# Optimization experiments

Hardware: AMD Instinct MI355X
Metric: run time of the kernel (lower is better)

## Reference

```python
import jax, jax.numpy as jnp
import numpy as np

B, L, HS, NWRD, NTGT, DIM = 8, 128, 1024, 32000, 2000, 128
EPS = 1e-12
T = 1.0  # eval temperature


def setup_inputs() -> dict:
    key = jax.random.key(0)
    ks = jax.random.split(key, 16)
    s = 0.02
    return {
        "inp_word": jax.random.randint(ks[0], (B, L), 0, NWRD, dtype=jnp.int32),
        "masks": jnp.ones((B, L), jnp.float32),
        "spt_mask": jax.random.randint(ks[1], (B, L), 0, 2, dtype=jnp.int32),
        "tgt_ids": jnp.sort(jax.random.randint(ks[2], (NTGT,), 0, NWRD, dtype=jnp.int32)),
        "ctx": jax.random.normal(ks[3], (B, L, HS), jnp.float32),
        "W_spt": jax.random.normal(ks[4], (HS, NTGT), jnp.float32) * s,
        "b_spt": jnp.zeros((NTGT,), jnp.float32),
        "W_nrm": jax.random.normal(ks[5], (HS, NWRD), jnp.float32) * s,
        "b_nrm": jnp.zeros((NWRD,), jnp.float32),
        "W_cpy": jax.random.normal(ks[6], (HS, HS), jnp.float32) * s,
        "b_cpy": jnp.zeros((HS,), jnp.float32),
        "word_emb": jax.random.normal(ks[7], (NWRD, DIM), jnp.float32) * s,
        "word_emb_tgt": jax.random.normal(ks[8], (NTGT, DIM), jnp.float32) * s,
        "g_spt": jax.random.gumbel(ks[9], (B, L, NTGT), jnp.float32),
        "g_nrm": jax.random.gumbel(ks[10], (B, L, NWRD + 1), jnp.float32),
    }


def reference(inp_word, masks, spt_mask, tgt_ids, ctx, W_spt, b_spt, W_nrm, b_nrm,
              W_cpy, b_cpy, word_emb, word_emb_tgt, g_spt, g_nrm):
    spt = spt_mask.astype(jnp.float32)                       # keyword tokens
    nrm = (1.0 - spt) * masks                                # normal (non-pad) tokens

    # special-token head: log(softmax + eps)
    pspt = jnp.log(jax.nn.softmax(jnp.einsum('blh,ht->blt', ctx, W_spt) + b_spt, axis=-1) + EPS)

    # normal head: vocab logits + self copy-attention score
    logits_nrm = jnp.einsum('blh,hv->blv', ctx, W_nrm) + b_nrm           # [B,L,NWRD]
    pcpy = jnp.einsum('blh,blh->bl', jnp.einsum('blh,hk->blk', ctx, W_cpy) + b_cpy, ctx)
    pnrm = jnp.log(jax.nn.softmax(jnp.concatenate([logits_nrm, pcpy[..., None]], axis=-1), axis=-1) + EPS)

    # gumbel-softmax relaxed samples
    sft_spt = jax.nn.softmax((pspt + g_spt) / T, axis=-1)    # [B,L,NTGT]
    sft_nrm = jax.nn.softmax((pnrm + g_nrm) / T, axis=-1)    # [B,L,NWRD+1]

    # hard word choices
    yspt = tgt_ids[jnp.argmax(sft_spt, axis=-1)]
    ynrm_raw = jnp.argmax(sft_nrm, axis=-1).astype(jnp.int32)
    ynrm = jnp.where(ynrm_raw == NWRD, inp_word, ynrm_raw)   # copy fallback
    obf_word = jnp.where(spt > 0, yspt, jnp.where(nrm > 0, ynrm, inp_word))

    # blended embeddings, scatter-combined per token group
    spt_emb = jnp.einsum('blt,td->bld', sft_spt, word_emb_tgt)
    nrm_emb = word_emb[inp_word] * sft_nrm[..., -1:] \
        + jnp.einsum('blv,vd->bld', sft_nrm[..., :-1], word_emb)
    base_emb = word_emb[obf_word]
    obf_word_emb = jnp.where(spt[..., None] > 0, spt_emb,
                             jnp.where(nrm[..., None] > 0, nrm_emb, base_emb))
    return obf_word_emb, obf_word, spt
```

## Files before the change

### kernel.cpp

```cpp
#include <hip/hip_runtime.h>
#include <math.h>

#define TOK   1024
#define HSZ   1024
#define DIM   128
#define NWRDC 32000
#define NTGTC 2000

typedef __attribute__((ext_vector_type(8))) short bf16x8;
typedef __attribute__((ext_vector_type(4))) float f32x4;

__device__ __forceinline__ ushort f2bf(float x) {
    union { float f; uint u; } c; c.f = x;
    return (ushort)((c.u + 0x7fffu + ((c.u >> 16) & 1u)) >> 16);
}
__device__ __forceinline__ float bf2f(ushort h) {
    union { uint u; float f; } c; c.u = ((uint)h) << 16;
    return c.f;
}
__device__ __forceinline__ uint4 pk8(const ushort v[8]) {
    uint4 u;
    u.x = (uint)v[0] | ((uint)v[1] << 16);
    u.y = (uint)v[2] | ((uint)v[3] << 16);
    u.z = (uint)v[4] | ((uint)v[5] << 16);
    u.w = (uint)v[6] | ((uint)v[7] << 16);
    return u;
}

#define GLL16(SRC, DST) __builtin_amdgcn_global_load_lds( \
    (const __attribute__((address_space(1))) void*)(SRC), \
    (__attribute__((address_space(3))) void*)(DST), 16, 0, 0)

__global__ __launch_bounds__(256) void split_ctx3(
    const float* __restrict__ x, ushort* __restrict__ hp,
    ushort* __restrict__ mp, ushort* __restrict__ lp)
{
    const int i4 = (blockIdx.x * 256 + threadIdx.x) * 4;
    float4 v = *(const float4*)(x + i4);
    float xs[4] = {v.x, v.y, v.z, v.w};
    ushort hh[4], mm[4], ll[4];
    #pragma unroll
    for (int k = 0; k < 4; ++k) {
        ushort h = f2bf(xs[k]);
        float r1 = xs[k] - bf2f(h);
        ushort m = f2bf(r1);
        ushort l = f2bf(r1 - bf2f(m));
        hh[k] = h; mm[k] = m; ll[k] = l;
    }
    uint2 u;
    u.x = (uint)hh[0] | ((uint)hh[1] << 16); u.y = (uint)hh[2] | ((uint)hh[3] << 16);
    *(uint2*)(hp + i4) = u;
    u.x = (uint)mm[0] | ((uint)mm[1] << 16); u.y = (uint)mm[2] | ((uint)mm[3] << 16);
    *(uint2*)(mp + i4) = u;
    u.x = (uint)ll[0] | ((uint)ll[1] << 16); u.y = (uint)ll[2] | ((uint)ll[3] << 16);
    *(uint2*)(lp + i4) = u;
}

__global__ __launch_bounds__(256, 2) void gemm_cpy(
    const ushort* __restrict__ ahi, const ushort* __restrict__ amd,
    const ushort* __restrict__ alo, const float* __restrict__ W,
    float* __restrict__ C)
{
    __shared__ __align__(16) ushort sm[30720];
    ushort* Ah = sm;
    ushort* Am = sm + 5120;
    ushort* Al = sm + 10240;
    ushort* Bh = sm + 15360;
    ushort* Bm = sm + 20480;
    ushort* Bl = sm + 25600;

    const int tid  = threadIdx.x;
    const int lane = tid & 63;
    const int fr   = lane & 15;
    const int fg   = lane >> 4;
    const int w    = tid >> 6;
    const int wrow = w >> 1;
    const int wcol = w & 1;
    const int t0   = blockIdx.x * 128;
    const int c0   = blockIdx.y * 128;

    const int arow = tid >> 2, akc = tid & 3;
    const int bcol = tid & 127, bkc0 = tid >> 7;

    f32x4 zero4 = {0.f, 0.f, 0.f, 0.f};
    f32x4 acc[4][4];
    #pragma unroll
    for (int i = 0; i < 4; ++i)
        #pragma unroll
        for (int j = 0; j < 4; ++j) acc[i][j] = zero4;

    for (int h0 = 0; h0 < HSZ; h0 += 32) {
        uint4 aH[2], aM[2], aL[2];
        float bx[2][8];
        #pragma unroll
        for (int rr = 0; rr < 2; ++rr) {
            const size_t so = (size_t)(t0 + arow + rr * 64) * HSZ + h0 + akc * 8;
            aH[rr] = *(const uint4*)(ahi + so);
            aM[rr] = *(const uint4*)(amd + so);
            aL[rr] = *(const uint4*)(alo + so);
        }
        #pragma unroll
        for (int rr = 0; rr < 2; ++rr) {
            const int kc = bkc0 + rr * 2;
            const float* wp = W + (size_t)(h0 + kc * 8) * HSZ + c0 + bcol;
            #pragma unroll
            for (int j = 0; j < 8; ++j) bx[rr][j] = wp[(size_t)j * HSZ];
        }
        __syncthreads();
        #pragma unroll
        for (int rr = 0; rr < 2; ++rr) {
            const int row = arow + rr * 64;
            *(uint4*)(Ah + row * 40 + akc * 8) = aH[rr];
            *(uint4*)(Am + row * 40 + akc * 8) = aM[rr];
            *(uint4*)(Al + row * 40 + akc * 8) = aL[rr];
        }
        #pragma unroll
        for (int rr = 0; rr < 2; ++rr) {
            const int kc = bkc0 + rr * 2;
            ushort hh[8], mm[8], ll[8];
            #pragma unroll
            for (int j = 0; j < 8; ++j) {
                float x = bx[rr][j];
                ushort h = f2bf(x);
                float r1 = x - bf2f(h);
                ushort m = f2bf(r1);
                hh[j] = h; mm[j] = m; ll[j] = f2bf(r1 - bf2f(m));
            }
            *(uint4*)(Bh + bcol * 40 + kc * 8) = pk8(hh);
            *(uint4*)(Bm + bcol * 40 + kc * 8) = pk8(mm);
            *(uint4*)(Bl + bcol * 40 + kc * 8) = pk8(ll);
        }
        __syncthreads();
        bf16x8 a1[4], a2[4], a3[4];
        #pragma unroll
        for (int i = 0; i < 4; ++i) {
            const int row = wrow * 64 + i * 16 + fr;
            a1[i] = *(const bf16x8*)(Ah + row * 40 + fg * 8);
            a2[i] = *(const bf16x8*)(Am + row * 40 + fg * 8);
            a3[i] = *(const bf16x8*)(Al + row * 40 + fg * 8);
        }
        #pragma unroll
        for (int j = 0; j < 4; ++j) {
            const int cr = wcol * 64 + j * 16 + fr;
            bf16x8 b1 = *(const bf16x8*)(Bh + cr * 40 + fg * 8);
            bf16x8 b2 = *(const bf16x8*)(Bm + cr * 40 + fg * 8);
            bf16x8 b3 = *(const bf16x8*)(Bl + cr * 40 + fg * 8);
            #pragma unroll
            for (int i = 0; i < 4; ++i) {
                acc[i][j] = __builtin_amdgcn_mfma_f32_16x16x32_bf16(a1[i], b1, acc[i][j], 0, 0, 0);
                acc[i][j] = __builtin_amdgcn_mfma_f32_16x16x32_bf16(a1[i], b2, acc[i][j], 0, 0, 0);
                acc[i][j] = __builtin_amdgcn_mfma_f32_16x16x32_bf16(a2[i], b1, acc[i][j], 0, 0, 0);
                acc[i][j] = __builtin_amdgcn_mfma_f32_16x16x32_bf16(a1[i], b3, acc[i][j], 0, 0, 0);
                acc[i][j] = __builtin_amdgcn_mfma_f32_16x16x32_bf16(a3[i], b1, acc[i][j], 0, 0, 0);
                acc[i][j] = __builtin_amdgcn_mfma_f32_16x16x32_bf16(a2[i], b2, acc[i][j], 0, 0, 0);
            }
        }
    }
    #pragma unroll
    for (int i = 0; i < 4; ++i)
        #pragma unroll
        for (int j = 0; j < 4; ++j)
            #pragma unroll
            for (int r = 0; r < 4; ++r) {
                const int trow = wrow * 64 + i * 16 + fg * 4 + r;
                const int dd   = wcol * 64 + j * 16 + fr;
                C[(size_t)(t0 + trow) * HSZ + c0 + dd] = acc[i][j][r];
            }
}

__global__ __launch_bounds__(256) void pcpy_dot(
    const float* __restrict__ C, const float* __restrict__ ctx,
    const float* __restrict__ bc, float* __restrict__ out)
{
    const int t = blockIdx.x, tid = threadIdx.x;
    const float4 c4 = *(const float4*)(C + (size_t)t * HSZ + tid * 4);
    const float4 x4 = *(const float4*)(ctx + (size_t)t * HSZ + tid * 4);
    const float4 b4 = *(const float4*)(bc + tid * 4);
    float p = (c4.x + b4.x) * x4.x + (c4.y + b4.y) * x4.y
            + (c4.z + b4.z) * x4.z + (c4.w + b4.w) * x4.w;
    #pragma unroll
    for (int off = 32; off > 0; off >>= 1) p += __shfl_down(p, off, 64);
    __shared__ float r4[4];
    if ((tid & 63) == 0) r4[tid >> 6] = p;
    __syncthreads();
    if (tid == 0) out[t] = r4[0] + r4[1] + r4[2] + r4[3];
}

__global__ __launch_bounds__(256, 2) void head_mfma(
    const ushort* __restrict__ ctx_hi, const ushort* __restrict__ ctx_lo,
    const float* __restrict__ W, const float* __restrict__ bias,
    const float* __restrict__ g, const float* __restrict__ emb,
    int V, int ldg, int tps, int n_tiles,
    float* __restrict__ wsW, float* __restrict__ wsBV,
    int* __restrict__ wsBI, float* __restrict__ wsE)
{
    __shared__ __align__(16) char smem[56320];
    ushort* Pl = (ushort*)smem;
    ushort* EM = (ushort*)(smem + 34816);
    float* sm_wsum = (float*)(smem + 53248);
    float* sm_bval = (float*)(smem + 54272);
    int*   sm_bidx = (int*)(smem + 55296);

    const int tid  = threadIdx.x;
    const int lane = tid & 63;
    const int fr   = lane & 15;
    const int fg   = lane >> 4;
    const int wv   = tid >> 6;
    const int wrow = wv >> 1;
    const int wcol = wv & 1;
    const int split = (int)blockIdx.x;
    const int t0    = (int)blockIdx.y * 128;

    if (tid < 128) {
        sm_wsum[tid * 2] = 0.f;        sm_wsum[tid * 2 + 1] = 0.f;
        sm_bval[tid * 2] = -INFINITY;  sm_bval[tid * 2 + 1] = -INFINITY;
        sm_bidx[tid * 2] = 0;          sm_bidx[tid * 2 + 1] = 0;
    }

    const int chunkRd  = (((fr & 1) << 2) | fg) ^ ((fr >> 1) & 7);
    const int laneAoff = wrow * 4096 + (fr >> 1) * 128 + chunkRd * 16;
    const int laneBoff = wcol * 4096 + (fr >> 1) * 128 + chunkRd * 16;

    const int cfA   = (lane & 7) ^ (lane >> 3);
    const int glTok = (wv * 8 + (lane >> 3)) * 2 + (cfA >> 2);
    const int glK   = (cfA & 3) * 8;
    const int glDst = wv * 1024;

    const int c4 = (tid & 31) * 4;
    const int hb = (tid >> 5) * 2;
    int wb01[4], wb23[4];
    #pragma unroll
    for (int i = 0; i < 4; ++i) {
        const int col = c4 + i;
        const int pair = col >> 1;
        const int ch01 = (((col & 1) << 2) | (hb >> 3)) ^ (pair & 7);
        const int ch23 = (((col & 1) << 2) | (2 + (hb >> 3))) ^ (pair & 7);
        wb01[i] = pair * 128 + ch01 * 16 + (hb & 7) * 2;
        wb23[i] = pair * 128 + ch23 * 16 + (hb & 7) * 2;
    }

    f32x4 zero4 = {0.f, 0.f, 0.f, 0.f};
    f32x4 Eacc[4][4];
    #pragma unroll
    for (int i = 0; i < 4; ++i)
        #pragma unroll
        for (int j = 0; j < 4; ++j) Eacc[i][j] = zero4;

    int tbeg = split * tps;
    int tend = tbeg + tps; if (tend > n_tiles) tend = n_tiles;

    #define STAGE_A(STEP, BASE) do {                                              \
        const size_t ro_ = (size_t)(t0 + glTok) * HSZ + (size_t)(STEP) * 32 + glK; \
        GLL16(ctx_hi + ro_,          (BASE) + glDst);                              \
        GLL16(ctx_hi + ro_ + 65536,  (BASE) + 4096 + glDst);                       \
        GLL16(ctx_lo + ro_,          (BASE) + 8192 + glDst);                       \
        GLL16(ctx_lo + ro_ + 65536,  (BASE) + 12288 + glDst);                      \
    } while (0)

    #define LOAD_W(STEP, VV) do {                                                 \
        const int gc_ = c0 + c4;                                                  \
        if (gc_ + 3 < V) {                                                        \
            const float* p_ = W + (size_t)((STEP) * 32 + hb) * V + gc_;           \
            VV[0] = *(const float4*)p_;                                           \
            VV[1] = *(const float4*)(p_ + V);                                     \
            VV[2] = *(const float4*)(p_ + 16 * (size_t)V);                        \
            VV[3] = *(const float4*)(p_ + 17 * (size_t)V);                        \
        } else {                                                                  \
            float4 z_ = {0.f, 0.f, 0.f, 0.f};                                     \
            VV[0] = z_; VV[1] = z_; VV[2] = z_; VV[3] = z_;                       \
        }                                                                         \
    } while (0)

    #define CONV_W(VV) do {                                                       \
        _Pragma("unroll")                                                         \
        for (int i_ = 0; i_ < 4; ++i_) {                                          \
            const float* fv0 = (const float*)&VV[0];                              \
            const float* fv1 = (const float*)&VV[1];                              \
            const float* fv2 = (const float*)&VV[2];                              \
            const float* fv3 = (const float*)&VV[3];                              \
            float a0 = fv0[i_], a1 = fv1[i_], a2 = fv2[i_], a3 = fv3[i_];         \
            ushort h0b = f2bf(a0); ushort l0b = f2bf(a0 - bf2f(h0b));             \
            ushort h1b = f2bf(a1); ushort l1b = f2bf(a1 - bf2f(h1b));             \
            ushort h2b = f2bf(a2); ushort l2b = f2bf(a2 - bf2f(h2b));             \
            ushort h3b = f2bf(a3); ushort l3b = f2bf(a3 - bf2f(h3b));             \
            *(uint*)(smem + 32768 + wb01[i_]) = (uint)h0b | ((uint)h1b << 16);    \
            *(uint*)(smem + 32768 + wb23[i_]) = (uint)h2b | ((uint)h3b << 16);    \
            *(uint*)(smem + 40960 + wb01[i_]) = (uint)l0b | ((uint)l1b << 16);    \
            *(uint*)(smem + 40960 + wb23[i_]) = (uint)l2b | ((uint)l3b << 16);    \
        }                                                                         \
    } while (0)

    for (int tt = tbeg; tt < tend; ++tt) {
        const int c0 = tt * 128;
        f32x4 acc[4][4];
        #pragma unroll
        for (int i = 0; i < 4; ++i)
            #pragma unroll
            for (int j = 0; j < 4; ++j) acc[i][j] = zero4;

        STAGE_A(0, smem);
        {
            float4 v0[4];
            LOAD_W(0, v0);
            CONV_W(v0);
        }
        __syncthreads();

        for (int ks = 0; ks < 32; ++ks) {
            const int cur = ks & 1;
            const bool more = (ks + 1) < 32;
            float4 vn[4];
            if (more) {
                STAGE_A(ks + 1, smem + (cur ^ 1) * 16384);
                LOAD_W(ks + 1, vn);
            }
            char* bA = smem + cur * 16384;
            bf16x8 ah[4], al[4];
            #pragma unroll
            for (int i = 0; i < 4; ++i) {
                ah[i] = *(const bf16x8*)(bA + laneAoff + i * 1024);
                al[i] = *(const bf16x8*)(bA + 8192 + laneAoff + i * 1024);
            }
            #pragma unroll
            for (int j = 0; j < 4; ++j) {
                bf16x8 vbh = *(const bf16x8*)(smem + 32768 + laneBoff + j * 1024);
                bf16x8 vbl = *(const bf16x8*)(smem + 40960 + laneBoff + j * 1024);
                #pragma unroll
                for (int i = 0; i < 4; ++i) {
                    acc[i][j] = __builtin_amdgcn_mfma_f32_16x16x32_bf16(ah[i], vbh, acc[i][j], 0, 0, 0);
                    acc[i][j] = __builtin_amdgcn_mfma_f32_16x16x32_bf16(ah[i], vbl, acc[i][j], 0, 0, 0);
                    acc[i][j] = __builtin_amdgcn_mfma_f32_16x16x32_bf16(al[i], vbh, acc[i][j], 0, 0, 0);
                }
            }
            __syncthreads();
            if (more) {
                CONV_W(vn);
            }
            __syncthreads();
        }

        float bias4[4];
        #pragma unroll
        for (int j = 0; j < 4; ++j) {
            const int gc = c0 + wcol * 64 + j * 16 + fr;
            bias4[j] = (gc < V) ? bias[gc] : 0.f;
        }
        #pragma unroll
        for (int i = 0; i < 4; ++i) {
            #pragma unroll
            for (int r = 0; r < 4; ++r) {
                const int trow = wrow * 64 + i * 16 + fg * 4 + r;
                const float* gp = g + (size_t)(t0 + trow) * ldg + c0 + wcol * 64 + fr;
                float esum = 0.f, mx = -INFINITY;
                int mi = 0;
                #pragma unroll
                for (int j = 0; j < 4; ++j) {
                    const int gc = c0 + wcol * 64 + j * 16 + fr;
                    float e = 0.f;
                    if (gc < V) {
                        const float s = acc[i][j][r] + bias4[j] + gp[j * 16];
                        e = __expf(s);
                        esum += e;
                        if (s > mx) { mx = s; mi = gc; }
                    }
                    Pl[trow * 136 + wcol * 64 + j * 16 + fr] = f2bf(e);
                }
                #pragma unroll
                for (int off = 1; off < 16; off <<= 1) {
                    const float ov = __shfl_xor(mx, off, 64);
                    const int   oi = __shfl_xor(mi, off, 64);
                    esum += __shfl_xor(esum, off, 64);
                    if (ov > mx || (ov == mx && oi < mi)) { mx = ov; mi = oi; }
                }
                if (fr == 0) {
                    sm_wsum[trow * 2 + wcol] += esum;
                    const float cb = sm_bval[trow * 2 + wcol];
                    const int   ci = sm_bidx[trow * 2 + wcol];
                    if (mx > cb || (mx == cb && mi < ci)) {
                        sm_bval[trow * 2 + wcol] = mx;
                        sm_bidx[trow * 2 + wcol] = mi;
                    }
                }
            }
        }

        #pragma unroll
        for (int hf = 0; hf < 2; ++hf) {
            __syncthreads();
            #pragma unroll
            for (int rr = 0; rr < 4; ++rr) {
                const int task = tid + rr * 256;
                const int d = task & 127;
                const int cc = task >> 7;
                ushort o8[8];
                #pragma unroll
                for (int j = 0; j < 8; ++j) {
                    const int gc = c0 + hf * 64 + cc * 8 + j;
                    o8[j] = (gc < V) ? f2bf(emb[(size_t)gc * DIM + d]) : (ushort)0;
                }
                *(uint4*)(EM + d * 72 + cc * 8) = pk8(o8);
            }
            __syncthreads();
            #pragma unroll
            for (int ksb = 0; ksb < 2; ++ksb) {
                bf16x8 ap[4];
                #pragma unroll
                for (int i = 0; i < 4; ++i) {
                    const int row = wrow * 64 + i * 16 + fr;
                    ap[i] = *(const bf16x8*)(Pl + row * 136 + hf * 64 + ksb * 32 + fg * 8);
                }
                #pragma unroll
                for (int j = 0; j < 4; ++j) {
                    const int dd = wcol * 64 + j * 16 + fr;
                    bf16x8 eb = *(const bf16x8*)(EM + dd * 72 + ksb * 32 + fg * 8);
                    #pragma unroll
                    for (int i = 0; i < 4; ++i)
                        Eacc[i][j] = __builtin_amdgcn_mfma_f32_16x16x32_bf16(ap[i], eb, Eacc[i][j], 0, 0, 0);
                }
            }
        }
        __syncthreads();
    }

    __syncthreads();
    if (tid < 128) {
        const float wsv = sm_wsum[tid * 2] + sm_wsum[tid * 2 + 1];
        const float b0 = sm_bval[tid * 2], b1 = sm_bval[tid * 2 + 1];
        const int   i0 = sm_bidx[tid * 2], i1 = sm_bidx[tid * 2 + 1];
        float bv; int bi;
        if (b0 > b1 || (b0 == b1 && i0 < i1)) { bv = b0; bi = i0; }
        else                                   { bv = b1; bi = i1; }
        const size_t o = (size_t)split * TOK + t0 + tid;
        wsW[o] = wsv; wsBV[o] = bv; wsBI[o] = bi;
    }
    #pragma unroll
    for (int i = 0; i < 4; ++i)
        #pragma unroll
        for (int j = 0; j < 4; ++j)
            #pragma unroll
            for (int r = 0; r < 4; ++r) {
                const int trow = wrow * 64 + i * 16 + fg * 4 + r;
                const int dd   = wcol * 64 + j * 16 + fr;
                wsE[((size_t)split * TOK + t0 + trow) * DIM + dd] = Eacc[i][j][r];
            }
}

__global__ __launch_bounds__(128) void combine_kernel(
    const int* __restrict__ inp_word, const float* __restrict__ masks,
    const int* __restrict__ spt_mask, const int* __restrict__ tgt_ids,
    const float* __restrict__ word_emb, const float* __restrict__ pcpy,
    const float* __restrict__ g_nrm,
    const float* __restrict__ nW, const float* __restrict__ nBV,
    const int* __restrict__ nBI, const float* __restrict__ nE, int NVn,
    const float* __restrict__ sW, const float* __restrict__ sBV,
    const int* __restrict__ sBI, const float* __restrict__ sE, int NVs,
    float* __restrict__ out)
{
    const int t = (int)blockIdx.x;
    const int d = (int)threadIdx.x;

    float Wn = 0.f, En = 0.f, bv = -INFINITY; int bi = 0;
    for (int v = 0; v < NVn; ++v) {
        const size_t o = (size_t)v * TOK + t;
        Wn += nW[o];
        En += nE[o * DIM + d];
        const float vv = nBV[o]; const int ii = nBI[o];
        if (vv > bv || (vv == bv && ii < bi)) { bv = vv; bi = ii; }
    }
    const int iw = inp_word[t];
    const float sc = pcpy[t] + g_nrm[(size_t)t * (NWRDC + 1) + NWRDC];
    const float ec = __expf(sc);
    Wn += ec;
    En += ec * word_emb[(size_t)iw * DIM + d];
    const int ynrm = (sc > bv) ? iw : bi;

    float Ws = 0.f, Ese = 0.f, sv = -INFINITY; int si = 0;
    for (int v = 0; v < NVs; ++v) {
        const size_t o = (size_t)v * TOK + t;
        Ws += sW[o];
        Ese += sE[o * DIM + d];
        const float vv = sBV[o]; const int ii = sBI[o];
        if (vv > sv || (vv == sv && ii < si)) { sv = vv; si = ii; }
    }
    const int yspt = tgt_ids[si];

    const float sptf = (float)spt_mask[t];
    const float nrmf = (1.f - sptf) * masks[t];

    float eo; int obf;
    if (sptf > 0.f)      { eo = Ese / Ws; obf = yspt; }
    else if (nrmf > 0.f) { eo = En / Wn;  obf = ynrm; }
    else                 { obf = iw; eo = word_emb[(size_t)iw * DIM + d]; }

    out[(size_t)t * DIM + d] = eo;
    if (d == 0) {
        out[(size_t)TOK * DIM + t]       = (float)obf;
        out[(size_t)TOK * DIM + TOK + t] = sptf;
    }
}

extern "C" void kernel_launch(void* const* d_in, const int* in_sizes, int n_in,
                              void* d_out, int out_size, void* d_ws, size_t ws_size,
                              hipStream_t stream)
{
    const int*   inp_word = (const int*)d_in[0];
    const float* masks    = (const float*)d_in[1];
    const int*   spt_mask = (const int*)d_in[2];
    const int*   tgt_ids  = (const int*)d_in[3];
    const float* ctx      = (const float*)d_in[4];
    const float* W_spt    = (const float*)d_in[5];
    const float* b_spt    = (const float*)d_in[6];
    const float* W_nrm    = (const float*)d_in[7];
    const float* b_nrm    = (const float*)d_in[8];
    const float* W_cpy    = (const float*)d_in[9];
    const float* b_cpy    = (const float*)d_in[10];
    const float* word_emb = (const float*)d_in[11];
    const float* word_emb_tgt = (const float*)d_in[12];
    const float* g_spt    = (const float*)d_in[13];
    const float* g_nrm    = (const float*)d_in[14];
    float* out = (float*)d_out;

    char* wsb = (char*)d_ws;
    float*  pcpy = (float*)wsb;
    ushort* ctxh = (ushort*)(wsb + 4096);
    ushort* ctxm = (ushort*)(wsb + 4096 + 2097152);
    ushort* ctxl = (ushort*)(wsb + 4096 + 4194304);
    char*   region = wsb + 4096 + 6291456;
    float*  Cws = (float*)region;

    const size_t per_split = (size_t)TOK * (DIM + 3) * 4;
    size_t avail = (ws_size > 6295552) ? (ws_size - 6295552) / per_split : 0;
    int NVn, NVs;
    if      (avail >= 72) { NVn = 64; NVs = 8; }
    else if (avail >= 56) { NVn = 48; NVs = 8; }
    else if (avail >= 40) { NVn = 32; NVs = 8; }
    else if (avail >= 24) { NVn = 16; NVs = 8; }
    else if (avail >= 12) { NVn = 8;  NVs = 4; }
    else if (avail >= 3)  { NVn = (int)avail - 1; NVs = 1; }
    else                  { NVn = 1;  NVs = 1; }

    float* nW  = (float*)region;
    float* nBV = nW + (size_t)NVn * TOK;
    int*   nBI = (int*)(nBV + (size_t)NVn * TOK);
    float* nE  = (float*)(nBI + (size_t)NVn * TOK);
    float* sW  = nE + (size_t)NVn * TOK * DIM;
    float* sBV = sW + (size_t)NVs * TOK;
    int*   sBI = (int*)(sBV + (size_t)NVs * TOK);
    float* sE  = (float*)(sBI + (size_t)NVs * TOK);

    const int ntile_n = NWRDC / 128;
    const int tps_n = (ntile_n + NVn - 1) / NVn;
    const int ntile_s = (NTGTC + 127) / 128;
    const int tps_s = (ntile_s + NVs - 1) / NVs;

    split_ctx3<<<dim3(TOK * HSZ / 1024), dim3(256), 0, stream>>>(ctx, ctxh, ctxm, ctxl);
    gemm_cpy<<<dim3(8, 8), dim3(256), 0, stream>>>(ctxh, ctxm, ctxl, W_cpy, Cws);
    pcpy_dot<<<dim3(TOK), dim3(256), 0, stream>>>(Cws, ctx, b_cpy, pcpy);
    head_mfma<<<dim3(NVn, 8), dim3(256), 0, stream>>>(
        ctxh, ctxm, W_nrm, b_nrm, g_nrm, word_emb, NWRDC, NWRDC + 1,
        tps_n, ntile_n, nW, nBV, nBI, nE);
    head_mfma<<<dim3(NVs, 8), dim3(256), 0, stream>>>(
        ctxh, ctxm, W_spt, b_spt, g_spt, word_emb_tgt, NTGTC, NTGTC,
        tps_s, ntile_s, sW, sBV, sBI, sE);
    combine_kernel<<<dim3(TOK), dim3(128), 0, stream>>>(
        inp_word, masks, spt_mask, tgt_ids, word_emb, pcpy, g_nrm,
        nW, nBV, nBI, nE, NVn, sW, sBV, sBI, sE, NVs, out);
    (void)in_sizes; (void)n_in; (void)out_size;
}
```

Baseline: 827.7 us.

## Pre-transpose vocab weights to bf16 and rescore top-3 candidates exactly

Adds a conversion kernel that transposes W_nrm and W_spt into bf16 hi (and lo residual) buffers in workspace. The main head kernel now runs a single-pass bf16 MFMA GEMM, loading both operands directly into LDS instead of converting fp32 weights inside the loop. To recover argmax accuracy it tracks the top-3 candidates per token, and the combine kernel rescores them in double precision using the hi/lo split. This cuts the per-tile weight conversion and the split-precision MFMA work, at the cost of a large workspace and an extra conversion pass over the weights on every call.

```diff
diff --git a/kernel.cpp b/kernel.cpp
--- a/kernel.cpp
+++ b/kernel.cpp
@@ -25,6 +25,15 @@
     u.z = (uint)v[4] | ((uint)v[5] << 16);
     u.w = (uint)v[6] | ((uint)v[7] << 16);
     return u;
+}
+__device__ __forceinline__ void ins3(float v, int ix, float s[3], int ii[3]) {
+    if (v > s[0] || (v == s[0] && ix < ii[0])) {
+        s[2] = s[1]; ii[2] = ii[1]; s[1] = s[0]; ii[1] = ii[0]; s[0] = v; ii[0] = ix;
+    } else if (v > s[1] || (v == s[1] && ix < ii[1])) {
+        s[2] = s[1]; ii[2] = ii[1]; s[1] = v; ii[1] = ix;
+    } else if (v > s[2] || (v == s[2] && ix < ii[2])) {
+        s[2] = v; ii[2] = ix;
+    }
 }
 
 #define GLL16(SRC, DST) __builtin_amdgcn_global_load_lds( \
@@ -54,6 +63,35 @@
     *(uint2*)(mp + i4) = u;
     u.x = (uint)ll[0] | ((uint)ll[1] << 16); u.y = (uint)ll[2] | ((uint)ll[3] << 16);
     *(uint2*)(lp + i4) = u;
+}
+
+__global__ __launch_bounds__(256) void conv_wt(
+    const float* __restrict__ W, int V,
+    ushort* __restrict__ Wh, void* __restrict__ Wl, int lf32)
+{
+    const int col = blockIdx.x * 256 + threadIdx.x;
+    const int k0 = blockIdx.y * 128;
+    for (int kk = 0; kk < 128; kk += 8) {
+        ushort h8[8], l8[8]; float lf[8];
+        #pragma unroll
+        for (int q = 0; q < 8; ++q) {
+            float x = (col < V) ? W[(size_t)(k0 + kk + q) * V + col] : 0.f;
+            union { float f; uint u; } c; c.f = x;
+            ushort h = (ushort)(c.u >> 16);
+            union { uint u; float f; } th; th.u = (uint)h << 16;
+            float r = x - th.f;
+            h8[q] = h; lf[q] = r; l8[q] = f2bf(r);
+        }
+        *(uint4*)(Wh + (size_t)col * 1024 + k0 + kk) = pk8(h8);
+        if (lf32) {
+            float* wl = (float*)Wl + (size_t)col * 1024 + k0 + kk;
+            float4 a = {lf[0], lf[1], lf[2], lf[3]};
+            float4 b = {lf[4], lf[5], lf[6], lf[7]};
+            *(float4*)wl = a; *(float4*)(wl + 4) = b;
+        } else {
+            *(uint4*)((ushort*)Wl + (size_t)col * 1024 + k0 + kk) = pk8(l8);
+        }
+    }
 }
 
 __global__ __launch_bounds__(256, 2) void gemm_cpy(
@@ -186,7 +224,230 @@
     if (tid == 0) out[t] = r4[0] + r4[1] + r4[2] + r4[3];
 }
 
-__global__ __launch_bounds__(256, 2) void head_mfma(
+__global__ __launch_bounds__(256, 2) void head_pre(
+    const ushort* __restrict__ ctx_hi, const ushort* __restrict__ Wt,
+    const float* __restrict__ bias, const float* __restrict__ g,
+    const float* __restrict__ emb,
+    int V, int ldg, int tps, int n_tiles,
+    float* __restrict__ wsW, float* __restrict__ wsBV,
+    int* __restrict__ wsBI, float* __restrict__ wsE)
+{
+    __shared__ __align__(16) char smem[60416];
+    ushort* Pl = (ushort*)smem;
+    ushort* EM = (ushort*)(smem + 34816);
+    float* sm_wsum = (float*)(smem + 53248);
+    float* sm_bval = (float*)(smem + 54272);
+    int*   sm_bidx = (int*)(smem + 57344);
+
+    const int tid  = threadIdx.x;
+    const int lane = tid & 63;
+    const int fr   = lane & 15;
+    const int fg   = lane >> 4;
+    const int wv   = tid >> 6;
+    const int wrow = wv >> 1;
+    const int wcol = wv & 1;
+    const int split = (int)blockIdx.x;
+    const int t0    = (int)blockIdx.y * 128;
+
+    if (tid < 128) {
+        sm_wsum[tid * 2] = 0.f; sm_wsum[tid * 2 + 1] = 0.f;
+        #pragma unroll
+        for (int s = 0; s < 3; ++s) {
+            sm_bval[(tid * 2) * 3 + s] = -INFINITY;
+            sm_bval[(tid * 2 + 1) * 3 + s] = -INFINITY;
+            sm_bidx[(tid * 2) * 3 + s] = 0;
+            sm_bidx[(tid * 2 + 1) * 3 + s] = 0;
+        }
+    }
+
+    const int chunkRd0 = (((fr & 1) << 2) | fg) ^ ((fr >> 1) & 7);
+    int aRd[4], bRd[4];
+    #pragma unroll
+    for (int i = 0; i < 4; ++i) {
+        aRd[i] = wrow * 4096 + i * 1024 + (fr >> 1) * 128 + ((chunkRd0 ^ i) << 4);
+        bRd[i] = wcol * 4096 + i * 1024 + (fr >> 1) * 128 + ((chunkRd0 ^ i) << 4);
+    }
+
+    const int v_ = (lane & 7) ^ (lane >> 3) ^ (wv & 3);
+    int rowq[2];
+    #pragma unroll
+    for (int q = 0; q < 2; ++q)
+        rowq[q] = 2 * (q * 32 + wv * 8 + (lane >> 3)) + (v_ >> 2);
+    const int glK = (v_ & 3) * 8;
+    const size_t srcA0 = (size_t)(t0 + rowq[0]) * HSZ + glK;
+    const size_t srcA1 = (size_t)(t0 + rowq[1]) * HSZ + glK;
+    const int dA0 = wv * 1024, dA1 = 4096 + wv * 1024;
+
+    f32x4 zero4 = {0.f, 0.f, 0.f, 0.f};
+    f32x4 Eacc[4][4];
+    #pragma unroll
+    for (int i = 0; i < 4; ++i)
+        #pragma unroll
+        for (int j = 0; j < 4; ++j) Eacc[i][j] = zero4;
+
+    int tbeg = split * tps;
+    int tend = tbeg + tps; if (tend > n_tiles) tend = n_tiles;
+
+    for (int tt = tbeg; tt < tend; ++tt) {
+        const int c0 = tt * 128;
+        const size_t srcB0 = (size_t)(c0 + rowq[0]) * HSZ + glK;
+        const size_t srcB1 = (size_t)(c0 + rowq[1]) * HSZ + glK;
+        f32x4 acc[4][4];
+        #pragma unroll
+        for (int i = 0; i < 4; ++i)
+            #pragma unroll
+            for (int j = 0; j < 4; ++j) acc[i][j] = zero4;
+
+        GLL16(ctx_hi + srcA0, smem + dA0);
+        GLL16(ctx_hi + srcA1, smem + dA1);
+        GLL16(Wt + srcB0, smem + 16384 + dA0);
+        GLL16(Wt + srcB1, smem + 16384 + dA1);
+        __syncthreads();
+
+        for (int ks = 0; ks < 32; ++ks) {
+            const int cur = ks & 1;
+            if (ks < 31) {
+                const int so = (ks + 1) * 32;
+                char* an = smem + (cur ^ 1) * 8192;
+                char* bn = smem + 16384 + (cur ^ 1) * 8192;
+                GLL16(ctx_hi + srcA0 + so, an + dA0);
+                GLL16(ctx_hi + srcA1 + so, an + dA1);
+                GLL16(Wt + srcB0 + so, bn + dA0);
+                GLL16(Wt + srcB1 + so, bn + dA1);
+            }
+            char* bA = smem + cur * 8192;
+            char* bB = smem + 16384 + cur * 8192;
+            bf16x8 ah[4], bh[4];
+            #pragma unroll
+            for (int i = 0; i < 4; ++i) ah[i] = *(const bf16x8*)(bA + aRd[i]);
+            #pragma unroll
+            for (int j = 0; j < 4; ++j) bh[j] = *(const bf16x8*)(bB + bRd[j]);
+            #pragma unroll
+            for (int j = 0; j < 4; ++j)
+                #pragma unroll
+                for (int i = 0; i < 4; ++i)
+                    acc[i][j] = __builtin_amdgcn_mfma_f32_16x16x32_bf16(ah[i], bh[j], acc[i][j], 0, 0, 0);
+            __syncthreads();
+        }
+
+        float bias4[4];
+        #pragma unroll
+        for (int j = 0; j < 4; ++j) {
+            const int gc = c0 + wcol * 64 + j * 16 + fr;
+            bias4[j] = (gc < V) ? bias[gc] : 0.f;
+        }
+        #pragma unroll
+        for (int i = 0; i < 4; ++i) {
+            #pragma unroll
+            for (int r = 0; r < 4; ++r) {
+                const int trow = wrow * 64 + i * 16 + fg * 4 + r;
+                const float* gp = g + (size_t)(t0 + trow) * ldg + c0 + wcol * 64 + fr;
+                float esum = 0.f;
+                float t3v[3] = {-INFINITY, -INFINITY, -INFINITY};
+                int   t3i[3] = {0, 0, 0};
+                #pragma unroll
+                for (int j = 0; j < 4; ++j) {
+                    const int gc = c0 + wcol * 64 + j * 16 + fr;
+                    float e = 0.f;
+                    if (gc < V) {
+                        const float s = acc[i][j][r] + bias4[j] + gp[j * 16];
+                        e = __expf(s);
+                        esum += e;
+                        ins3(s, gc, t3v, t3i);
+                    }
+                    Pl[trow * 136 + wcol * 64 + j * 16 + fr] = f2bf(e);
+                }
+                #pragma unroll
+                for (int off = 1; off < 16; off <<= 1) {
+                    float o0 = __shfl_xor(t3v[0], off, 64);
+                    float o1 = __shfl_xor(t3v[1], off, 64);
+                    float o2 = __shfl_xor(t3v[2], off, 64);
+                    int q0 = __shfl_xor(t3i[0], off, 64);
+                    int q1 = __shfl_xor(t3i[1], off, 64);
+                    int q2 = __shfl_xor(t3i[2], off, 64);
+                    esum += __shfl_xor(esum, off, 64);
+                    ins3(o0, q0, t3v, t3i);
+                    ins3(o1, q1, t3v, t3i);
+                    ins3(o2, q2, t3v, t3i);
+                }
+                if (fr == 0) {
+                    const int sb = (trow * 2 + wcol) * 3;
+                    sm_wsum[trow * 2 + wcol] += esum;
+                    float sh[3] = {sm_bval[sb], sm_bval[sb + 1], sm_bval[sb + 2]};
+                    int shi[3] = {sm_bidx[sb], sm_bidx[sb + 1], sm_bidx[sb + 2]};
+                    ins3(t3v[0], t3i[0], sh, shi);
+                    ins3(t3v[1], t3i[1], sh, shi);
+                    ins3(t3v[2], t3i[2], sh, shi);
+                    sm_bval[sb] = sh[0]; sm_bval[sb + 1] = sh[1]; sm_bval[sb + 2] = sh[2];
+                    sm_bidx[sb] = shi[0]; sm_bidx[sb + 1] = shi[1]; sm_bidx[sb + 2] = shi[2];
+                }
+            }
+        }
+
+        #pragma unroll
+        for (int hf = 0; hf < 2; ++hf) {
+            __syncthreads();
+            #pragma unroll
+            for (int rr = 0; rr < 4; ++rr) {
+                const int task = tid + rr * 256;
+                const int dd0 = task & 127;
+                const int cc = task >> 7;
+                ushort o8[8];
+                #pragma unroll
+                for (int j = 0; j < 8; ++j) {
+                    const int gc = c0 + hf * 64 + cc * 8 + j;
+                    o8[j] = (gc < V) ? f2bf(emb[(size_t)gc * DIM + dd0]) : (ushort)0;
+                }
+                *(uint4*)(EM + dd0 * 72 + cc * 8) = pk8(o8);
+            }
+            __syncthreads();
+            #pragma unroll
+            for (int ksb = 0; ksb < 2; ++ksb) {
+                bf16x8 ap[4];
+                #pragma unroll
+                for (int i = 0; i < 4; ++i) {
+                    const int row = wrow * 64 + i * 16 + fr;
+                    ap[i] = *(const bf16x8*)(Pl + row * 136 + hf * 64 + ksb * 32 + fg * 8);
+                }
+                #pragma unroll
+                for (int j = 0; j < 4; ++j) {
+                    const int dd = wcol * 64 + j * 16 + fr;
+                    bf16x8 eb = *(const bf16x8*)(EM + dd * 72 + ksb * 32 + fg * 8);
+                    #pragma unroll
+                    for (int i = 0; i < 4; ++i)
+                        Eacc[i][j] = __builtin_amdgcn_mfma_f32_16x16x32_bf16(ap[i], eb, Eacc[i][j], 0, 0, 0);
+                }
+            }
+        }
+        __syncthreads();
+    }
+
+    __syncthreads();
+    if (tid < 128) {
+        const int sb0 = (tid * 2) * 3, sb1 = (tid * 2 + 1) * 3;
+        float v3[3] = {sm_bval[sb0], sm_bval[sb0 + 1], sm_bval[sb0 + 2]};
+        int i3[3] = {sm_bidx[sb0], sm_bidx[sb0 + 1], sm_bidx[sb0 + 2]};
+        ins3(sm_bval[sb1], sm_bidx[sb1], v3, i3);
+        ins3(sm_bval[sb1 + 1], sm_bidx[sb1 + 1], v3, i3);
+        ins3(sm_bval[sb1 + 2], sm_bidx[sb1 + 2], v3, i3);
+        const size_t o = (size_t)split * TOK + t0 + tid;
+        wsW[o] = sm_wsum[tid * 2] + sm_wsum[tid * 2 + 1];
+        #pragma unroll
+        for (int s = 0; s < 3; ++s) { wsBV[o * 3 + s] = v3[s]; wsBI[o * 3 + s] = i3[s]; }
+    }
+    #pragma unroll
+    for (int i = 0; i < 4; ++i)
+        #pragma unroll
+        for (int j = 0; j < 4; ++j)
+            #pragma unroll
+            for (int r = 0; r < 4; ++r) {
+                const int trow = wrow * 64 + i * 16 + fg * 4 + r;
+                const int dd   = wcol * 64 + j * 16 + fr;
+                wsE[((size_t)split * TOK + t0 + trow) * DIM + dd] = Eacc[i][j][r];
+            }
+}
+
+__global__ __launch_bounds__(256, 2) void head_fb(
     const ushort* __restrict__ ctx_hi, const ushort* __restrict__ ctx_lo,
     const float* __restrict__ W, const float* __restrict__ bias,
     const float* __restrict__ g, const float* __restrict__ emb,
@@ -249,7 +510,7 @@
     int tbeg = split * tps;
     int tend = tbeg + tps; if (tend > n_tiles) tend = n_tiles;
 
-    #define STAGE_A(STEP, BASE) do {                                              \
+    #define STAGE_A(STEP, BASE) do {                                               \
         const size_t ro_ = (size_t)(t0 + glTok) * HSZ + (size_t)(STEP) * 32 + glK; \
         GLL16(ctx_hi + ro_,          (BASE) + glDst);                              \
         GLL16(ctx_hi + ro_ + 65536,  (BASE) + 4096 + glDst);                       \
@@ -258,36 +519,36 @@
     } while (0)
 
     #define LOAD_W(STEP, VV) do {                                                 \
-        const int gc_ = c0 + c4;                                                  \
-        if (gc_ + 3 < V) {                                                        \
-            const float* p_ = W + (size_t)((STEP) * 32 + hb) * V + gc_;           \
-            VV[0] = *(const float4*)p_;                                           \
-            VV[1] = *(const float4*)(p_ + V);                                     \
-            VV[2] = *(const float4*)(p_ + 16 * (size_t)V);                        \
-            VV[3] = *(const float4*)(p_ + 17 * (size_t)V);                        \
-        } else {                                                                  \
-            float4 z_ = {0.f, 0.f, 0.f, 0.f};                                     \
-            VV[0] = z_; VV[1] = z_; VV[2] = z_; VV[3] = z_;                       \
-        }                                                                         \
+        const int gc_ = c0 + c4;                                                   \
+        if (gc_ + 3 < V) {                                                         \
+            const float* p_ = W + (size_t)((STEP) * 32 + hb) * V + gc_;            \
+            VV[0] = *(const float4*)p_;                                            \
+            VV[1] = *(const float4*)(p_ + V);                                      \
+            VV[2] = *(const float4*)(p_ + 16 * (size_t)V);                         \
+            VV[3] = *(const float4*)(p_ + 17 * (size_t)V);                         \
+        } else {                                                                   \
+            float4 z_ = {0.f, 0.f, 0.f, 0.f};                                      \
+            VV[0] = z_; VV[1] = z_; VV[2] = z_; VV[3] = z_;                        \
+        }                                                                          \
     } while (0)
 
     #define CONV_W(VV) do {                                                       \
-        _Pragma("unroll")                                                         \
-        for (int i_ = 0; i_ < 4; ++i_) {                                          \
-            const float* fv0 = (const float*)&VV[0];                              \
-            const float* fv1 = (const float*)&VV[1];                              \
-            const float* fv2 = (const float*)&VV[2];                              \
-            const float* fv3 = (const float*)&VV[3];                              \
-            float a0 = fv0[i_], a1 = fv1[i_], a2 = fv2[i_], a3 = fv3[i_];         \
-            ushort h0b = f2bf(a0); ushort l0b = f2bf(a0 - bf2f(h0b));             \
-            ushort h1b = f2bf(a1); ushort l1b = f2bf(a1 - bf2f(h1b));             \
-            ushort h2b = f2bf(a2); ushort l2b = f2bf(a2 - bf2f(h2b));             \
-            ushort h3b = f2bf(a3); ushort l3b = f2bf(a3 - bf2f(h3b));             \
-            *(uint*)(smem + 32768 + wb01[i_]) = (uint)h0b | ((uint)h1b << 16);    \
-            *(uint*)(smem + 32768 + wb23[i_]) = (uint)h2b | ((uint)h3b << 16);    \
-            *(uint*)(smem + 40960 + wb01[i_]) = (uint)l0b | ((uint)l1b << 16);    \
-            *(uint*)(smem + 40960 + wb23[i_]) = (uint)l2b | ((uint)l3b << 16);    \
-        }                                                                         \
+        _Pragma("unroll")                                                          \
+        for (int i_ = 0; i_ < 4; ++i_) {                                           \
+            const float* fv0 = (const float*)&VV[0];                               \
+            const float* fv1 = (const float*)&VV[1];                               \
+            const float* fv2 = (const float*)&VV[2];                               \
+            const float* fv3 = (const float*)&VV[3];                               \
+            float a0 = fv0[i_], a1 = fv1[i_], a2 = fv2[i_], a3 = fv3[i_];          \
+            ushort h0b = f2bf(a0); ushort l0b = f2bf(a0 - bf2f(h0b));              \
+            ushort h1b = f2bf(a1); ushort l1b = f2bf(a1 - bf2f(h1b));              \
+            ushort h2b = f2bf(a2); ushort l2b = f2bf(a2 - bf2f(h2b));              \
+            ushort h3b = f2bf(a3); ushort l3b = f2bf(a3 - bf2f(h3b));              \
+            *(uint*)(smem + 32768 + wb01[i_]) = (uint)h0b | ((uint)h1b << 16);     \
+            *(uint*)(smem + 32768 + wb23[i_]) = (uint)h2b | ((uint)h3b << 16);     \
+            *(uint*)(smem + 40960 + wb01[i_]) = (uint)l0b | ((uint)l1b << 16);     \
+            *(uint*)(smem + 40960 + wb23[i_]) = (uint)l2b | ((uint)l3b << 16);     \
+        }                                                                          \
     } while (0)
 
     for (int tt = tbeg; tt < tend; ++tt) {
@@ -333,9 +594,7 @@
                 }
             }
             __syncthreads();
-            if (more) {
-                CONV_W(vn);
-            }
+            if (more) CONV_W(vn);
             __syncthreads();
         }
 
@@ -390,15 +649,15 @@
             #pragma unroll
             for (int rr = 0; rr < 4; ++rr) {
                 const int task = tid + rr * 256;
-                const int d = task & 127;
+                const int dd0 = task & 127;
                 const int cc = task >> 7;
                 ushort o8[8];
                 #pragma unroll
                 for (int j = 0; j < 8; ++j) {
                     const int gc = c0 + hf * 64 + cc * 8 + j;
-                    o8[j] = (gc < V) ? f2bf(emb[(size_t)gc * DIM + d]) : (ushort)0;
-                }
-                *(uint4*)(EM + d * 72 + cc * 8) = pk8(o8);
+                    o8[j] = (gc < V) ? f2bf(emb[(size_t)gc * DIM + dd0]) : (ushort)0;
+                }
+                *(uint4*)(EM + dd0 * 72 + cc * 8) = pk8(o8);
             }
             __syncthreads();
             #pragma unroll
@@ -431,7 +690,9 @@
         if (b0 > b1 || (b0 == b1 && i0 < i1)) { bv = b0; bi = i0; }
         else                                   { bv = b1; bi = i1; }
         const size_t o = (size_t)split * TOK + t0 + tid;
-        wsW[o] = wsv; wsBV[o] = bv; wsBI[o] = bi;
+        wsW[o] = wsv;
+        wsBV[o * 3] = bv; wsBV[o * 3 + 1] = -INFINITY; wsBV[o * 3 + 2] = -INFINITY;
+        wsBI[o * 3] = bi; wsBI[o * 3 + 1] = 0; wsBI[o * 3 + 2] = 0;
     }
     #pragma unroll
     for (int i = 0; i < 4; ++i)
@@ -443,53 +704,143 @@
                 const int dd   = wcol * 64 + j * 16 + fr;
                 wsE[((size_t)split * TOK + t0 + trow) * DIM + dd] = Eacc[i][j][r];
             }
-}
-
-__global__ __launch_bounds__(128) void combine_kernel(
+    #undef STAGE_A
+    #undef LOAD_W
+    #undef CONV_W
+}
+
+__global__ __launch_bounds__(128) void combine2(
     const int* __restrict__ inp_word, const float* __restrict__ masks,
     const int* __restrict__ spt_mask, const int* __restrict__ tgt_ids,
     const float* __restrict__ word_emb, const float* __restrict__ pcpy,
-    const float* __restrict__ g_nrm,
+    const float* __restrict__ g_nrm, const float* __restrict__ g_spt,
+    const float* __restrict__ ctx,
+    const float* __restrict__ b_nrm, const float* __restrict__ b_spt,
+    const ushort* __restrict__ WtNh, const void* __restrict__ WtNl,
+    const ushort* __restrict__ WtSh, const void* __restrict__ WtSl,
     const float* __restrict__ nW, const float* __restrict__ nBV,
     const int* __restrict__ nBI, const float* __restrict__ nE, int NVn,
     const float* __restrict__ sW, const float* __restrict__ sBV,
     const int* __restrict__ sBI, const float* __restrict__ sE, int NVs,
-    float* __restrict__ out)
+    float* __restrict__ out, int recomp, int lf32)
 {
+    __shared__ double sred[2][6];
+    __shared__ float sfin[6];
     const int t = (int)blockIdx.x;
     const int d = (int)threadIdx.x;
 
-    float Wn = 0.f, En = 0.f, bv = -INFINITY; int bi = 0;
+    float Wn = 0.f, En = 0.f;
+    float cv[3] = {-INFINITY, -INFINITY, -INFINITY}; int ci[3] = {0, 0, 0};
     for (int v = 0; v < NVn; ++v) {
         const size_t o = (size_t)v * TOK + t;
         Wn += nW[o];
         En += nE[o * DIM + d];
-        const float vv = nBV[o]; const int ii = nBI[o];
-        if (vv > bv || (vv == bv && ii < bi)) { bv = vv; bi = ii; }
-    }
+        #pragma unroll
+        for (int s = 0; s < 3; ++s) ins3(nBV[o * 3 + s], nBI[o * 3 + s], cv, ci);
+    }
+    float Ws = 0.f, Es = 0.f;
+    float dv[3] = {-INFINITY, -INFINITY, -INFINITY}; int di[3] = {0, 0, 0};
+    for (int v = 0; v < NVs; ++v) {
+        const size_t o = (size_t)v * TOK + t;
+        Ws += sW[o];
+        Es += sE[o * DIM + d];
+        #pragma unroll
+        for (int s = 0; s < 3; ++s) ins3(sBV[o * 3 + s], sBI[o * 3 + s], dv, di);
+    }
+
+    float bnv, bsv; int bni, bsi;
+    if (recomp) {
+        float cxv[8];
+        #pragma unroll
+        for (int q = 0; q < 8; ++q) cxv[q] = ctx[(size_t)t * HSZ + d * 8 + q];
+        double part[6] = {0, 0, 0, 0, 0, 0};
+        #pragma unroll
+        for (int c = 0; c < 3; ++c) {
+            if (cv[c] > -1e30f) {
+                const ushort* ph = WtNh + (size_t)ci[c] * HSZ + d * 8;
+                double p = 0.0;
+                if (lf32) {
+                    const float* pl = (const float*)WtNl + (size_t)ci[c] * HSZ + d * 8;
+                    #pragma unroll
+                    for (int q = 0; q < 8; ++q)
+                        p += (double)cxv[q] * ((double)bf2f(ph[q]) + (double)pl[q]);
+                } else {
+                    const ushort* pl = (const ushort*)WtNl + (size_t)ci[c] * HSZ + d * 8;
+                    #pragma unroll
+                    for (int q = 0; q < 8; ++q)
+                        p += (double)cxv[q] * ((double)bf2f(ph[q]) + (double)bf2f(pl[q]));
+                }
+                part[c] = p;
+            }
+        }
+        #pragma unroll
+        for (int c = 0; c < 3; ++c) {
+            if (dv[c] > -1e30f) {
+                const ushort* ph = WtSh + (size_t)di[c] * HSZ + d * 8;
+                double p = 0.0;
+                if (lf32) {
+                    const float* pl = (const float*)WtSl + (size_t)di[c] * HSZ + d * 8;
+                    #pragma unroll
+                    for (int q = 0; q < 8; ++q)
+                        p += (double)cxv[q] * ((double)bf2f(ph[q]) + (double)pl[q]);
+                } else {
+                    const ushort* pl = (const ushort*)WtSl + (size_t)di[c] * HSZ + d * 8;
+                    #pragma unroll
+                    for (int q = 0; q < 8; ++q)
+                        p += (double)cxv[q] * ((double)bf2f(ph[q]) + (double)bf2f(pl[q]));
+                }
+                part[3 + c] = p;
+            }
+        }
+        #pragma unroll
+        for (int c = 0; c < 6; ++c)
+            for (int off = 32; off > 0; off >>= 1)
+                part[c] += __shfl_down(part[c], off, 64);
+        if ((d & 63) == 0) {
+            #pragma unroll
+            for (int c = 0; c < 6; ++c) sred[d >> 6][c] = part[c];
+        }
+        __syncthreads();
+        if (d == 0) {
+            #pragma unroll
+            for (int c = 0; c < 3; ++c) {
+                sfin[c] = (cv[c] > -1e30f)
+                    ? (float)(sred[0][c] + sred[1][c]) + b_nrm[ci[c]]
+                      + g_nrm[(size_t)t * (NWRDC + 1) + ci[c]]
+                    : -INFINITY;
+                sfin[3 + c] = (dv[c] > -1e30f)
+                    ? (float)(sred[0][3 + c] + sred[1][3 + c]) + b_spt[di[c]]
+                      + g_spt[(size_t)t * NTGTC + di[c]]
+                    : -INFINITY;
+            }
+        }
+        __syncthreads();
+        bnv = sfin[0]; bni = ci[0];
+        #pragma unroll
+        for (int c = 1; c < 3; ++c)
+            if (sfin[c] > bnv || (sfin[c] == bnv && ci[c] < bni)) { bnv = sfin[c]; bni = ci[c]; }
+        bsv = sfin[3]; bsi = di[0];
+        #pragma unroll
+        for (int c = 1; c < 3; ++c)
+            if (sfin[3 + c] > bsv || (sfin[3 + c] == bsv && di[c] < bsi)) { bsv = sfin[3 + c]; bsi = di[c]; }
+    } else {
+        bnv = cv[0]; bni = ci[0]; bsv = dv[0]; bsi = di[0];
+    }
+
     const int iw = inp_word[t];
     const float sc = pcpy[t] + g_nrm[(size_t)t * (NWRDC + 1) + NWRDC];
     const float ec = __expf(sc);
     Wn += ec;
     En += ec * word_emb[(size_t)iw * DIM + d];
-    const int ynrm = (sc > bv) ? iw : bi;
-
-    float Ws = 0.f, Ese = 0.f, sv = -INFINITY; int si = 0;
-    for (int v = 0; v < NVs; ++v) {
-        const size_t o = (size_t)v * TOK + t;
-        Ws += sW[o];
-        Ese += sE[o * DIM + d];
-        const float vv = sBV[o]; const int ii = sBI[o];
-        if (vv > sv || (vv == sv && ii < si)) { sv = vv; si = ii; }
-    }
-    const int yspt = tgt_ids[si];
+    const int ynrm = (sc > bnv) ? iw : bni;
+    const int yspt = tgt_ids[bsi];
 
     const float sptf = (float)spt_mask[t];
     const float nrmf = (1.f - sptf) * masks[t];
 
     float eo; int obf;
-    if (sptf > 0.f)      { eo = Ese / Ws; obf = yspt; }
-    else if (nrmf > 0.f) { eo = En / Wn;  obf = ynrm; }
+    if (sptf > 0.f)      { eo = Es / Ws; obf = yspt; }
+    else if (nrmf > 0.f) { eo = En / Wn; obf = ynrm; }
     else                 { obf = iw; eo = word_emb[(size_t)iw * DIM + d]; }
 
     out[(size_t)t * DIM + d] = eo;
@@ -521,49 +872,94 @@
     float* out = (float*)d_out;
 
     char* wsb = (char*)d_ws;
+    const size_t O_CTXH = 4096;
+    const size_t O_CTXM = 4096 + 2097152;
+    const size_t O_CTXL = 4096 + 4194304;
+    const size_t O_WTNH = 6295552;
+    const size_t O_WTSH = 71831552;
+    const size_t O_L    = 76025856;
+    const size_t per_split = 552960;
+
+    struct Pair { int n, s; };
+    const Pair pairs[] = {{64,8},{48,8},{32,8},{24,8},{16,8},{8,4},{4,2},{2,1},{1,1}};
+    auto pick = [&](size_t base, int& NVn, int& NVs) -> bool {
+        for (int pi = 0; pi < 9; ++pi) {
+            size_t reg = (size_t)(pairs[pi].n + pairs[pi].s) * per_split;
+            if (reg < 4194304) reg = 4194304;
+            if (ws_size >= base + reg) { NVn = pairs[pi].n; NVs = pairs[pi].s; return true; }
+        }
+        return false;
+    };
+
+    int mode = 0, NVn = 1, NVs = 1;
+    size_t region_off = 6295552;
+    int nvn2, nvs2, nvn1, nvs1;
+    bool f2 = pick(215486464, nvn2, nvs2);
+    bool f1 = pick(145756160, nvn1, nvs1);
+    if (f2 && nvn2 >= 16)      { mode = 2; NVn = nvn2; NVs = nvs2; region_off = 215486464; }
+    else if (f1 && nvn1 >= 16) { mode = 1; NVn = nvn1; NVs = nvs1; region_off = 145756160; }
+    else if (f2)               { mode = 2; NVn = nvn2; NVs = nvs2; region_off = 215486464; }
+    else if (f1)               { mode = 1; NVn = nvn1; NVs = nvs1; region_off = 145756160; }
+    else {
+        mode = 0; region_off = 6295552;
+        size_t avail = (ws_size > 6295552) ? (ws_size - 6295552) : 0;
+        NVn = 1; NVs = 1;
+        for (int pi = 0; pi < 9; ++pi) {
+            size_t reg = (size_t)(pairs[pi].n + pairs[pi].s) * per_split;
+            if (reg < 4194304) reg = 4194304;
+            if (avail >= reg) { NVn = pairs[pi].n; NVs = pairs[pi].s; break; }
+        }
+    }
+
     float*  pcpy = (float*)wsb;
-    ushort* ctxh = (ushort*)(wsb + 4096);
-    ushort* ctxm = (ushort*)(wsb + 4096 + 2097152);
-    ushort* ctxl = (ushort*)(wsb + 4096 + 4194304);
-    char*   region = wsb + 4096 + 6291456;
-    float*  Cws = (float*)region;
-
-    const size_t per_split = (size_t)TOK * (DIM + 3) * 4;
-    size_t avail = (ws_size > 6295552) ? (ws_size - 6295552) / per_split : 0;
-    int NVn, NVs;
-    if      (avail >= 72) { NVn = 64; NVs = 8; }
-    else if (avail >= 56) { NVn = 48; NVs = 8; }
-    else if (avail >= 40) { NVn = 32; NVs = 8; }
-    else if (avail >= 24) { NVn = 16; NVs = 8; }
-    else if (avail >= 12) { NVn = 8;  NVs = 4; }
-    else if (avail >= 3)  { NVn = (int)avail - 1; NVs = 1; }
-    else                  { NVn = 1;  NVs = 1; }
+    ushort* ctxh = (ushort*)(wsb + O_CTXH);
+    ushort* ctxm = (ushort*)(wsb + O_CTXM);
+    ushort* ctxl = (ushort*)(wsb + O_CTXL);
+    ushort* WtNh = (ushort*)(wsb + O_WTNH);
+    ushort* WtSh = (ushort*)(wsb + O_WTSH);
+    void* WtNl = (void*)(wsb + O_L);
+    void* WtSl = (mode == 2) ? (void*)(wsb + 207097856) : (void*)(wsb + 141561856);
+    char* region = wsb + region_off;
+    float* Cws = (float*)region;
 
     float* nW  = (float*)region;
     float* nBV = nW + (size_t)NVn * TOK;
-    int*   nBI = (int*)(nBV + (size_t)NVn * TOK);
-    float* nE  = (float*)(nBI + (size_t)NVn * TOK);
+    int*   nBI = (int*)(nBV + (size_t)NVn * TOK * 3);
+    float* nE  = (float*)(nBI + (size_t)NVn * TOK * 3);
     float* sW  = nE + (size_t)NVn * TOK * DIM;
     float* sBV = sW + (size_t)NVs * TOK;
-    int*   sBI = (int*)(sBV + (size_t)NVs * TOK);
-    float* sE  = (float*)(sBI + (size_t)NVs * TOK);
-
-    const int ntile_n = NWRDC / 128;
-    const int tps_n = (ntile_n + NVn - 1) / NVn;
-    const int ntile_s = (NTGTC + 127) / 128;
-    const int tps_s = (ntile_s + NVs - 1) / NVs;
+    int*   sBI = (int*)(sBV + (size_t)NVs * TOK * 3);
+    float* sE  = (float*)(sBI + (size_t)NVs * TOK * 3);
+
+    const int tps_n = (250 + NVn - 1) / NVn;
+    const int tps_s = (16 + NVs - 1) / NVs;
 
     split_ctx3<<<dim3(TOK * HSZ / 1024), dim3(256), 0, stream>>>(ctx, ctxh, ctxm, ctxl);
+    if (mode >= 1) {
+        conv_wt<<<dim3(125, 8), dim3(256), 0, stream>>>(W_nrm, NWRDC, WtNh, WtNl, mode == 2);
+        conv_wt<<<dim3(8, 8), dim3(256), 0, stream>>>(W_spt, NTGTC, WtSh, WtSl, mode == 2);
+    }
     gemm_cpy<<<dim3(8, 8), dim3(256), 0, stream>>>(ctxh, ctxm, ctxl, W_cpy, Cws);
     pcpy_dot<<<dim3(TOK), dim3(256), 0, stream>>>(Cws, ctx, b_cpy, pcpy);
-    head_mfma<<<dim3(NVn, 8), dim3(256), 0, stream>>>(
-        ctxh, ctxm, W_nrm, b_nrm, g_nrm, word_emb, NWRDC, NWRDC + 1,
-        tps_n, ntile_n, nW, nBV, nBI, nE);
-    head_mfma<<<dim3(NVs, 8), dim3(256), 0, stream>>>(
-        ctxh, ctxm, W_spt, b_spt, g_spt, word_emb_tgt, NTGTC, NTGTC,
-        tps_s, ntile_s, sW, sBV, sBI, sE);
-    combine_kernel<<<dim3(TOK), dim3(128), 0, stream>>>(
-        inp_word, masks, spt_mask, tgt_ids, word_emb, pcpy, g_nrm,
-        nW, nBV, nBI, nE, NVn, sW, sBV, sBI, sE, NVs, out);
+    if (mode >= 1) {
+        head_pre<<<dim3(NVn, 8), dim3(256), 0, stream>>>(
+            ctxh, WtNh, b_nrm, g_nrm, word_emb, NWRDC, NWRDC + 1,
+            tps_n, 250, nW, nBV, nBI, nE);
+        head_pre<<<dim3(NVs, 8), dim3(256), 0, stream>>>(
+            ctxh, WtSh, b_spt, g_spt, word_emb_tgt, NTGTC, NTGTC,
+            tps_s, 16, sW, sBV, sBI, sE);
+    } else {
+        head_fb<<<dim3(NVn, 8), dim3(256), 0, stream>>>(
+            ctxh, ctxm, W_nrm, b_nrm, g_nrm, word_emb, NWRDC, NWRDC + 1,
+            tps_n, 250, nW, nBV, nBI, nE);
+        head_fb<<<dim3(NVs, 8), dim3(256), 0, stream>>>(
+            ctxh, ctxm, W_spt, b_spt, g_spt, word_emb_tgt, NTGTC, NTGTC,
+            tps_s, 16, sW, sBV, sBI, sE);
+    }
+    combine2<<<dim3(TOK), dim3(128), 0, stream>>>(
+        inp_word, masks, spt_mask, tgt_ids, word_emb, pcpy, g_nrm, g_spt, ctx,
+        b_nrm, b_spt, WtNh, WtNl, WtSh, WtSl,
+        nW, nBV, nBI, nE, NVn, sW, sBV, sBI, sE, NVs,
+        out, mode >= 1 ? 1 : 0, mode == 2 ? 1 : 0);
     (void)in_sizes; (void)n_in; (void)out_size;
 }
```

Result: slower. 1.675 ms (+102.3%).
